# Kernel optimization log

Measured on AMD Instinct MI355X. Metric: run time of the kernel, lower is better.

## Reference

```python
import jax, jax.numpy as jnp
import numpy as np

NUM_NODES = 102400
NUM_EDGES = 3276800
NUM_GRAPHS = 1024
LAMBDA_MAX = 2.0


def setup_inputs() -> dict:
    key = jax.random.key(0)
    ks = jax.random.split(key, 12)
    inp = {}
    inp['x'] = jax.random.normal(ks[0], (NUM_NODES, 128), dtype=jnp.float32)
    inp['edge_index'] = jax.random.randint(ks[1], (2, NUM_EDGES), 0, NUM_NODES, dtype=jnp.int32).astype(jnp.int64)
    inp['edge_attr'] = jax.random.uniform(ks[2], (NUM_EDGES,), dtype=jnp.float32)
    inp['batch'] = jnp.sort(jax.random.randint(ks[3], (NUM_NODES,), 0, NUM_GRAPHS, dtype=jnp.int32).astype(jnp.int64))
    inp['w1'] = jax.random.normal(ks[4], (3, 128, 64), dtype=jnp.float32) * 0.05
    inp['b1'] = jax.random.normal(ks[5], (64,), dtype=jnp.float32) * 0.05
    inp['w2'] = jax.random.normal(ks[6], (3, 64, 64), dtype=jnp.float32) * 0.05
    inp['b2'] = jax.random.normal(ks[7], (64,), dtype=jnp.float32) * 0.05
    inp['w3'] = jax.random.normal(ks[8], (3, 64, 128), dtype=jnp.float32) * 0.05
    inp['b3'] = jax.random.normal(ks[9], (128,), dtype=jnp.float32) * 0.05
    inp['lin_w'] = jax.random.normal(ks[10], (128, 2), dtype=jnp.float32) * 0.05
    inp['lin_b'] = jax.random.normal(ks[11], (2,), dtype=jnp.float32) * 0.05
    return inp


def _cheb_norm(edge_index, edge_attr, num_nodes):
    # PyG ChebConv.__norm__ with normalization='sym', lambda_max=2.0:
    #   L = I - D^{-1/2} A D^{-1/2};  Lhat = (2/lambda_max) * L - I
    # off-diagonal weights: -(2/lmax) * d_i^{-1/2} w_ij d_j^{-1/2}
    # diagonal coefficient:  (2/lmax) - 1  (== 0 for lmax = 2)
    src, dst = edge_index[0], edge_index[1]
    deg = jax.ops.segment_sum(edge_attr, src, num_segments=num_nodes)
    dinv = jnp.where(deg > 0, jax.lax.rsqrt(jnp.where(deg > 0, deg, 1.0)), 0.0)
    w = -(2.0 / LAMBDA_MAX) * dinv[src] * edge_attr * dinv[dst]
    diag = (2.0 / LAMBDA_MAX) - 1.0
    return w, diag


def _cheb_conv(x, src, dst, norm_w, diag, weight, bias):
    # weight: [K, Fin, Fout]; Chebyshev recurrence T0=x, T1=Lhat x, Tk=2 Lhat T_{k-1} - T_{k-2}
    n = x.shape[0]

    def spmv(v):  # Lhat @ v via edge-list scatter/gather
        return jax.ops.segment_sum(norm_w[:, None] * v[src], dst, num_segments=n) + diag * v

    Tx0 = x
    out = Tx0 @ weight[0]
    Tx1 = spmv(Tx0)
    out = out + Tx1 @ weight[1]
    for k in range(2, weight.shape[0]):
        Tx2 = 2.0 * spmv(Tx1) - Tx0
        out = out + Tx2 @ weight[k]
        Tx0, Tx1 = Tx1, Tx2
    return out + bias


def reference(x, edge_index, edge_attr, batch, w1, b1, w2, b2, w3, b3, lin_w, lin_b):
    n = x.shape[0]
    src, dst = edge_index[0], edge_index[1]
    norm_w, diag = _cheb_norm(edge_index, edge_attr, n)
    h = jax.nn.relu(_cheb_conv(x, src, dst, norm_w, diag, w1, b1))
    h = jax.nn.relu(_cheb_conv(h, src, dst, norm_w, diag, w2, b2))
    h = jax.nn.relu(_cheb_conv(h, src, dst, norm_w, diag, w3, b3))
    # global_mean_pool over graph ids
    sums = jax.ops.segment_sum(h, batch, num_segments=NUM_GRAPHS)
    cnts = jax.ops.segment_sum(jnp.ones((n,), h.dtype), batch, num_segments=NUM_GRAPHS)
    pooled = sums / jnp.maximum(cnts, 1.0)[:, None]
    return pooled @ lin_w + lin_b
```

## Files before the change

### kernel.cpp

```cpp
#include <hip/hip_runtime.h>
#include <cstddef>
#include <cstdint>

#define N_NODES 102400
#define N_EDGES 3276800
#define N_GRAPHS 1024
#define NBUCK 400
#define NBB 512
#define EPB 6400
#define MAXB 12288
#define N64 ((size_t)N_NODES * 64)

typedef unsigned short ushortT;
typedef unsigned int uintT;
typedef __attribute__((ext_vector_type(8))) short bf16x8;
typedef __attribute__((ext_vector_type(4))) float f32x4;

__device__ __forceinline__ float b2f(ushortT h) {
    return __uint_as_float(((uintT)h) << 16);
}
__device__ __forceinline__ ushortT f2b(float f) {
    uintT u = __float_as_uint(f);
    uintT r = (u + 0x7fffu + ((u >> 16) & 1u)) >> 16;
    return (ushortT)r;
}
__device__ __forceinline__ float loF(uintT w) { return __uint_as_float(w << 16); }
__device__ __forceinline__ float hiF(uintT w) { return __uint_as_float(w & 0xffff0000u); }

__global__ __launch_bounds__(256) void k_binA(const int* __restrict__ src,
                                              const int* __restrict__ dst,
                                              int* __restrict__ blkCntD,
                                              int* __restrict__ blkCntS) {
    __shared__ int hd[NBUCK], hs[NBUCK];
    int t = threadIdx.x;
    for (int i = t; i < NBUCK; i += 256) { hd[i] = 0; hs[i] = 0; }
    __syncthreads();
    int base = blockIdx.x * EPB;
    const int4* s4 = (const int4*)(src + base);
    const int4* d4 = (const int4*)(dst + base);
    for (int v = t; v < EPB / 4; v += 256) {
        int4 d = d4[v];
        int4 s = s4[v];
        atomicAdd(&hd[d.x >> 8], 1);
        atomicAdd(&hd[d.y >> 8], 1);
        atomicAdd(&hd[d.z >> 8], 1);
        atomicAdd(&hd[d.w >> 8], 1);
        atomicAdd(&hs[s.x >> 8], 1);
        atomicAdd(&hs[s.y >> 8], 1);
        atomicAdd(&hs[s.z >> 8], 1);
        atomicAdd(&hs[s.w >> 8], 1);
    }
    __syncthreads();
    for (int i = t; i < NBUCK; i += 256) {
        blkCntD[(size_t)blockIdx.x * NBUCK + i] = hd[i];
        blkCntS[(size_t)blockIdx.x * NBUCK + i] = hs[i];
    }
}

__global__ __launch_bounds__(256) void k_bbase(const int* __restrict__ blkCnt,
                                               int* __restrict__ blkRel,
                                               int* __restrict__ bucketTot) {
    __shared__ int sc[NBB];
    int b = blockIdx.x, t = threadIdx.x;
    int v0 = blkCnt[(size_t)t * NBUCK + b];
    int v1 = blkCnt[(size_t)(t + 256) * NBUCK + b];
    sc[t] = v0; sc[t + 256] = v1;
    __syncthreads();
    for (int o = 1; o < NBB; o <<= 1) {
        int x0 = (t >= o) ? sc[t - o] : 0;
        int x1 = (t + 256 >= o) ? sc[t + 256 - o] : 0;
        __syncthreads();
        sc[t] += x0; sc[t + 256] += x1;
        __syncthreads();
    }
    blkRel[(size_t)t * NBUCK + b] = sc[t] - v0;
    blkRel[(size_t)(t + 256) * NBUCK + b] = sc[t + 256] - v1;
    if (t == 255) bucketTot[b] = sc[NBB - 1];
}

__global__ void k_bscan(const int* __restrict__ bucketTotD,
                        const int* __restrict__ bucketTotS,
                        int* __restrict__ binBaseD,
                        int* __restrict__ binBaseS,
                        int* __restrict__ rowp) {
    int t = threadIdx.x;
    if (t == 0) {
        int run = 0;
        for (int i = 0; i < NBUCK; i++) { binBaseD[i] = run; run += bucketTotD[i]; }
        binBaseD[NBUCK] = run;
        rowp[N_NODES] = run;
    } else if (t == 64) {
        int run = 0;
        for (int i = 0; i < NBUCK; i++) { binBaseS[i] = run; run += bucketTotS[i]; }
        binBaseS[NBUCK] = run;
    }
}

__global__ __launch_bounds__(512) void k_binB2(const int* __restrict__ src,
                                               const int* __restrict__ dst,
                                               const float* __restrict__ attr,
                                               const int* __restrict__ blkCntD,
                                               const int* __restrict__ blkCntS,
                                               const int* __restrict__ blkRelD,
                                               const int* __restrict__ blkRelS,
                                               const int* __restrict__ binBaseD,
                                               const int* __restrict__ binBaseS,
                                               int2* __restrict__ edsD,
                                               int2* __restrict__ edsS) {
    __shared__ int sxD[EPB];
    __shared__ int syD[EPB];
    __shared__ ushortT spD[EPB];
    __shared__ int sxS[EPB];
    __shared__ int syS[EPB];
    __shared__ ushortT spS[EPB];
    __shared__ int lcurD[NBUCK], deltaD[NBUCK];
    __shared__ int lcurS[NBUCK], deltaS[NBUCK];
    int bx = blockIdx.x, t = threadIdx.x;

    int vD = (t < NBUCK) ? blkCntD[(size_t)bx * NBUCK + t] : 0;
    int vS = (t < NBUCK) ? blkCntS[(size_t)bx * NBUCK + t] : 0;
    sxD[t] = vD; sxS[t] = vS;
    __syncthreads();
    for (int o = 1; o < 512; o <<= 1) {
        int xD = (t >= o) ? sxD[t - o] : 0;
        int xS = (t >= o) ? sxS[t - o] : 0;
        __syncthreads();
        sxD[t] += xD; sxS[t] += xS;
        __syncthreads();
    }
    if (t < NBUCK) {
        int eD = sxD[t] - vD;
        lcurD[t] = eD;
        deltaD[t] = binBaseD[t] + blkRelD[(size_t)bx * NBUCK + t] - eD;
        int eS = sxS[t] - vS;
        lcurS[t] = eS;
        deltaS[t] = binBaseS[t] + blkRelS[(size_t)bx * NBUCK + t] - eS;
    }
    __syncthreads();

    int base = bx * EPB;
    for (int v = t; v < EPB / 2; v += 512) {
        int e0 = base + v * 2;
        int2 s2 = *(const int2*)(src + e0);
        int2 d2 = *(const int2*)(dst + e0);
        float2 a2 = *(const float2*)(attr + e0);
        int bkt, lp;
        bkt = d2.x >> 8;
        lp = atomicAdd(&lcurD[bkt], 1);
        spD[lp] = (ushortT)bkt; sxD[lp] = (s2.x << 8) | (d2.x & 255);
        syD[lp] = __float_as_int(a2.x);
        bkt = s2.x >> 8;
        lp = atomicAdd(&lcurS[bkt], 1);
        spS[lp] = (ushortT)bkt; sxS[lp] = s2.x & 255;
        syS[lp] = __float_as_int(a2.x);
        bkt = d2.y >> 8;
        lp = atomicAdd(&lcurD[bkt], 1);
        spD[lp] = (ushortT)bkt; sxD[lp] = (s2.y << 8) | (d2.y & 255);
        syD[lp] = __float_as_int(a2.y);
        bkt = s2.y >> 8;
        lp = atomicAdd(&lcurS[bkt], 1);
        spS[lp] = (ushortT)bkt; sxS[lp] = s2.y & 255;
        syS[lp] = __float_as_int(a2.y);
    }
    __syncthreads();
    for (int i = t; i < EPB; i += 512) {
        edsD[i + deltaD[spD[i]]] = make_int2(sxD[i], syD[i]);
        edsS[i + deltaS[spS[i]]] = make_int2(sxS[i], syS[i]);
    }
}

__global__ __launch_bounds__(256) void k_deg(const int2* __restrict__ edsS,
                                             const int* __restrict__ binBaseS,
                                             float* __restrict__ dinv) {
    __shared__ float degL[256];
    int b = blockIdx.x, t = threadIdx.x;
    degL[t] = 0.f;
    __syncthreads();
    int s0 = binBaseS[b], s1 = binBaseS[b + 1];
    for (int i = s0 + t; i < s1; i += 256) {
        int2 e = edsS[i];
        atomicAdd(&degL[e.x], __int_as_float(e.y));
    }
    __syncthreads();
    float d = degL[t];
    dinv[b * 256 + t] = d > 0.f ? rsqrtf(d) : 0.f;
}

__global__ __launch_bounds__(512) void k_csr(const int2* __restrict__ edsD,
                                             const int* __restrict__ binBaseD,
                                             const float* __restrict__ dinvG,
                                             int* __restrict__ rowp,
                                             int2* __restrict__ cedge) {
    __shared__ int cnt2[256 * 16];
    __shared__ int cntL[256];
    __shared__ float dL[256];
    __shared__ int2 st[MAXB];
    int b = blockIdx.x, t = threadIdx.x;
    for (int i = t; i < 256 * 16; i += 512) cnt2[i] = 0;
    if (t < 256) dL[t] = dinvG[b * 256 + t];
    __syncthreads();
    int s0 = binBaseD[b], s1 = binBaseD[b + 1];
    for (int i = s0 + t; i < s1; i += 512) {
        int2 e = edsD[i];
        atomicAdd(&cnt2[(e.x & 255) * 16 + ((e.x >> 8) >> 13)], 1);
    }
    __syncthreads();
    if (t < 256) {
        int run = 0;
#pragma unroll
        for (int o = 0; o < 16; o++) {
            int c = cnt2[t * 16 + o];
            cnt2[t * 16 + o] = run;
            run += c;
        }
        cntL[t] = run;
    }
    __syncthreads();
    int v = (t < 256) ? cntL[t] : 0;
    for (int o = 1; o < 256; o <<= 1) {
        int x = (t < 256 && t >= o) ? cntL[t - o] : 0;
        __syncthreads();
        if (t < 256) cntL[t] += x;
        __syncthreads();
    }
    if (t < 256) {
        int excl = cntL[t] - v;
        rowp[b * 256 + t] = s0 + excl;
#pragma unroll
        for (int o = 0; o < 16; o++) cnt2[t * 16 + o] += excl;
    }
    __syncthreads();
    for (int i = s0 + t; i < s1; i += 512) {
        int2 e = edsD[i];
        int dl = e.x & 255;
        int sg = e.x >> 8;
        float w = -__int_as_float(e.y) * dinvG[sg] * dL[dl];
        int p = atomicAdd(&cnt2[dl * 16 + (sg >> 13)], 1);
        st[p] = make_int2(sg, __float_as_int(w));
    }
    __syncthreads();
    int n = s1 - s0;
    for (int i = t; i < n; i += 512) cedge[s0 + i] = st[i];
}

__global__ __launch_bounds__(256) void k_cast(const float* __restrict__ x,
                                              ushortT* __restrict__ Xhi,
                                              ushortT* __restrict__ Xlo) {
    int i = blockIdx.x * 256 + threadIdx.x;
    int n = i >> 5;
    int kq = (i & 31) * 4;
    float4 v = ((const float4*)x)[i];
    int s = kq >> 6, kk = kq & 63;
    size_t o = (size_t)s * N64 + (size_t)n * 64 + kk;
    ushort4 h, l;
    h.x = f2b(v.x); l.x = f2b(v.x - b2f(h.x));
    h.y = f2b(v.y); l.y = f2b(v.y - b2f(h.y));
    h.z = f2b(v.z); l.z = f2b(v.z - b2f(h.z));
    h.w = f2b(v.w); l.w = f2b(v.w - b2f(h.w));
    *(ushort4*)(Xhi + o) = h;
    *(ushort4*)(Xlo + o) = l;
}

template <int L>
__global__ void k_wprep(const float* __restrict__ w, ushortT* __restrict__ Wth,
                        ushortT* __restrict__ Wtl) {
    int i = blockIdx.x * 256 + threadIdx.x;
    float v;
    if (L == 1) {
        if (i >= 192 * 128) return;
        int n = i / 128, k = i % 128;
        if (n < 64)       v = w[k * 64 + n] - w[16384 + k * 64 + n];
        else if (n < 128) v = w[8192 + k * 64 + (n - 64)];
        else              v = w[16384 + k * 64 + (n - 128)];
    } else if (L == 2) {
        if (i >= 192 * 64) return;
        int n = i / 64, k = i % 64;
        if (n < 64)       v = w[k * 64 + n] - w[8192 + k * 64 + n];
        else if (n < 128) v = w[4096 + k * 64 + (n - 64)];
        else              v = w[8192 + k * 64 + (n - 128)];
    } else {
        if (i >= 128 * 192) return;
        int n = i / 192, k = i % 192;
        v = w[(k >> 6) * 8192 + (k & 63) * 128 + n];
    }
    ushortT h = f2b(v);
    Wth[i] = h;
    Wtl[i] = f2b(v - b2f(h));
}

template <int KTOT, int NTOT, int MODE>
__global__ __launch_bounds__(512) void k_mgemm(
    const ushortT* __restrict__ Ah0, const ushortT* __restrict__ Ah1,
    const ushortT* __restrict__ Ah2, const ushortT* __restrict__ Al0,
    const ushortT* __restrict__ Al1, const ushortT* __restrict__ Al2,
    const ushortT* __restrict__ Wth, const ushortT* __restrict__ Wtl,
    const float* __restrict__ bias, float* __restrict__ outf,
    ushortT* __restrict__ outb) {
    constexpr int KPAD = 72;
    constexpr int NCT = NTOT / 16;
    __shared__ ushortT Bh[NTOT * KPAD];
    __shared__ ushortT Bl[NTOT * KPAD];
    const ushortT* Ah[3] = {Ah0, Ah1, Ah2};
    const ushortT* Al[3] = {Al0, Al1, Al2};
    int t = threadIdx.x;
    int lane = t & 63;
    int wv = t >> 6;
    int m = lane & 15, q = lane >> 4;
    int r0 = blockIdx.x * 256 + wv * 32;
    int ar0 = r0 + m;
    int ar1 = r0 + 16 + m;

    f32x4 acc[2][NCT];
#pragma unroll
    for (int rf = 0; rf < 2; rf++)
#pragma unroll
        for (int ct = 0; ct < NCT; ct++)
#pragma unroll
            for (int j = 0; j < 4; j++) acc[rf][ct][j] = 0.f;

#pragma unroll
    for (int kc = 0; kc < KTOT / 64; kc++) {
        __syncthreads();
        for (int i = t; i < NTOT * 8; i += 512) {
            int col = i >> 3, k = (i & 7) * 8;
            *(uint4*)(Bh + col * KPAD + k) =
                *(const uint4*)(Wth + (size_t)col * KTOT + kc * 64 + k);
            *(uint4*)(Bl + col * KPAD + k) =
                *(const uint4*)(Wtl + (size_t)col * KTOT + kc * 64 + k);
        }
        __syncthreads();
        const ushortT* Ahc = Ah[kc];
        const ushortT* Alc = Al[kc];
#pragma unroll
        for (int ks2 = 0; ks2 < 2; ks2++) {
            int kk = ks2 * 32 + q * 8;
            bf16x8 ah0 = *(const bf16x8*)(Ahc + (size_t)ar0 * 64 + kk);
            bf16x8 al0 = *(const bf16x8*)(Alc + (size_t)ar0 * 64 + kk);
            bf16x8 ah1 = *(const bf16x8*)(Ahc + (size_t)ar1 * 64 + kk);
            bf16x8 al1 = *(const bf16x8*)(Alc + (size_t)ar1 * 64 + kk);
#pragma unroll
            for (int ct = 0; ct < NCT; ct++) {
                int bo = (ct * 16 + m) * KPAD + ks2 * 32 + q * 8;
                bf16x8 bh = *(const bf16x8*)(Bh + bo);
                bf16x8 bl = *(const bf16x8*)(Bl + bo);
                acc[0][ct] = __builtin_amdgcn_mfma_f32_16x16x32_bf16(ah0, bh, acc[0][ct], 0, 0, 0);
                acc[0][ct] = __builtin_amdgcn_mfma_f32_16x16x32_bf16(al0, bh, acc[0][ct], 0, 0, 0);
                acc[0][ct] = __builtin_amdgcn_mfma_f32_16x16x32_bf16(ah0, bl, acc[0][ct], 0, 0, 0);
                acc[1][ct] = __builtin_amdgcn_mfma_f32_16x16x32_bf16(ah1, bh, acc[1][ct], 0, 0, 0);
                acc[1][ct] = __builtin_amdgcn_mfma_f32_16x16x32_bf16(al1, bh, acc[1][ct], 0, 0, 0);
                acc[1][ct] = __builtin_amdgcn_mfma_f32_16x16x32_bf16(ah1, bl, acc[1][ct], 0, 0, 0);
            }
        }
    }

#pragma unroll
    for (int rf = 0; rf < 2; rf++)
#pragma unroll
        for (int ct = 0; ct < NCT; ct++)
#pragma unroll
            for (int rg = 0; rg < 4; rg++) {
                int row = r0 + rf * 16 + q * 4 + rg;
                float v = acc[rf][ct][rg];
                if (MODE == 0) {
                    if (ct < 8)
                        outf[(size_t)row * 128 + ct * 16 + m] = v;
                    else
                        outb[(size_t)row * 64 + (ct - 8) * 16 + m] = f2b(v);
                } else {
                    int col = ct * 16 + m;
                    outf[(size_t)row * 128 + col] = fmaxf(v + bias[col], 0.f);
                }
            }
}

template <int MODE, int SA, bool AUXB, bool WLO>
__global__ __launch_bounds__(256) void k_spmm(const int* __restrict__ rowp,
                                              const int2* __restrict__ cedge,
                                              const ushortT* __restrict__ Xb,
                                              const float* __restrict__ auxF,
                                              const ushortT* __restrict__ auxH,
                                              const ushortT* __restrict__ auxL,
                                              const float* __restrict__ bias,
                                              ushortT* __restrict__ Yh,
                                              ushortT* __restrict__ Yl) {
    int node = blockIdx.x * 4 + (threadIdx.x >> 6);
    int lane = threadIdx.x & 63;
    int q = lane >> 3;
    int f = (lane & 7) * 8;
    int s = rowp[node], e = rowp[node + 1];
    const ushortT* Xf = Xb + f;
    float a0 = 0.f, a1 = 0.f, a2 = 0.f, a3 = 0.f;
    float a4 = 0.f, a5 = 0.f, a6 = 0.f, a7 = 0.f;
    for (int i = s; i < e; i += 16) {
        int i0 = min(i + q, e - 1);
        int i1 = min(i + 8 + q, e - 1);
        int2 ed0 = cedge[i0];
        int2 ed1 = cedge[i1];
        float w0 = (i + q < e) ? __int_as_float(ed0.y) : 0.f;
        float w1 = (i + 8 + q < e) ? __int_as_float(ed1.y) : 0.f;
        uint4 u0 = *(const uint4*)(Xf + ((size_t)ed0.x << 6));
        uint4 u1 = *(const uint4*)(Xf + ((size_t)ed1.x << 6));
        a0 = fmaf(w0, loF(u0.x), a0);
        a1 = fmaf(w0, hiF(u0.x), a1);
        a2 = fmaf(w0, loF(u0.y), a2);
        a3 = fmaf(w0, hiF(u0.y), a3);
        a4 = fmaf(w0, loF(u0.z), a4);
        a5 = fmaf(w0, hiF(u0.z), a5);
        a6 = fmaf(w0, loF(u0.w), a6);
        a7 = fmaf(w0, hiF(u0.w), a7);
        a0 = fmaf(w1, loF(u1.x), a0);
        a1 = fmaf(w1, hiF(u1.x), a1);
        a2 = fmaf(w1, loF(u1.y), a2);
        a3 = fmaf(w1, hiF(u1.y), a3);
        a4 = fmaf(w1, loF(u1.z), a4);
        a5 = fmaf(w1, hiF(u1.z), a5);
        a6 = fmaf(w1, loF(u1.w), a6);
        a7 = fmaf(w1, hiF(u1.w), a7);
    }
    a0 += __shfl_xor(a0, 8); a0 += __shfl_xor(a0, 16); a0 += __shfl_xor(a0, 32);
    a1 += __shfl_xor(a1, 8); a1 += __shfl_xor(a1, 16); a1 += __shfl_xor(a1, 32);
    a2 += __shfl_xor(a2, 8); a2 += __shfl_xor(a2, 16); a2 += __shfl_xor(a2, 32);
    a3 += __shfl_xor(a3, 8); a3 += __shfl_xor(a3, 16); a3 += __shfl_xor(a3, 32);
    a4 += __shfl_xor(a4, 8); a4 += __shfl_xor(a4, 16); a4 += __shfl_xor(a4, 32);
    a5 += __shfl_xor(a5, 8); a5 += __shfl_xor(a5, 16); a5 += __shfl_xor(a5, 32);
    a6 += __shfl_xor(a6, 8); a6 += __shfl_xor(a6, 16); a6 += __shfl_xor(a6, 32);
    a7 += __shfl_xor(a7, 8); a7 += __shfl_xor(a7, 16); a7 += __shfl_xor(a7, 32);

    if (q == 0 || (WLO && q == 1)) {
        float x0 = 0.f, x1 = 0.f, x2 = 0.f, x3 = 0.f;
        float x4 = 0.f, x5 = 0.f, x6 = 0.f, x7 = 0.f;
        if (MODE != 0) {
            if (AUXB) {
                uint4 ha = *(const uint4*)(auxH + (size_t)node * 64 + f);
                uint4 la = *(const uint4*)(auxL + (size_t)node * 64 + f);
                x0 = loF(ha.x) + loF(la.x);
                x1 = hiF(ha.x) + hiF(la.x);
                x2 = loF(ha.y) + loF(la.y);
                x3 = hiF(ha.y) + hiF(la.y);
                x4 = loF(ha.z) + loF(la.z);
                x5 = hiF(ha.z) + hiF(la.z);
                x6 = loF(ha.w) + loF(la.w);
                x7 = hiF(ha.w) + hiF(la.w);
            } else {
                float4 av0 = *(const float4*)(auxF + (size_t)node * SA + f);
                float4 av1 = *(const float4*)(auxF + (size_t)node * SA + f + 4);
                x0 = av0.x; x1 = av0.y; x2 = av0.z; x3 = av0.w;
                x4 = av1.x; x5 = av1.y; x6 = av1.z; x7 = av1.w;
            }
        }
        float r0, r1, r2, r3, r4, r5, r6, r7;
        if (MODE == 0) {
            r0 = a0; r1 = a1; r2 = a2; r3 = a3;
            r4 = a4; r5 = a5; r6 = a6; r7 = a7;
        } else if (MODE == 1) {
            r0 = x0 + 2.f * a0; r1 = x1 + 2.f * a1;
            r2 = x2 + 2.f * a2; r3 = x3 + 2.f * a3;
            r4 = x4 + 2.f * a4; r5 = x5 + 2.f * a5;
            r6 = x6 + 2.f * a6; r7 = x7 + 2.f * a7;
        } else if (MODE == 2) {
            r0 = 2.f * a0 - x0; r1 = 2.f * a1 - x1;
            r2 = 2.f * a2 - x2; r3 = 2.f * a3 - x3;
            r4 = 2.f * a4 - x4; r5 = 2.f * a5 - x5;
            r6 = 2.f * a6 - x6; r7 = 2.f * a7 - x7;
        } else {
            float4 bv0 = *(const float4*)(bias + f);
            float4 bv1 = *(const float4*)(bias + f + 4);
            r0 = fmaxf(x0 + a0 + bv0.x, 0.f);
            r1 = fmaxf(x1 + a1 + bv0.y, 0.f);
            r2 = fmaxf(x2 + a2 + bv0.z, 0.f);
            r3 = fmaxf(x3 + a3 + bv0.w, 0.f);
            r4 = fmaxf(x4 + a4 + bv1.x, 0.f);
            r5 = fmaxf(x5 + a5 + bv1.y, 0.f);
            r6 = fmaxf(x6 + a6 + bv1.z, 0.f);
            r7 = fmaxf(x7 + a7 + bv1.w, 0.f);
        }
        ushortT h0 = f2b(r0), h1 = f2b(r1), h2 = f2b(r2), h3 = f2b(r3);
        ushortT h4 = f2b(r4), h5 = f2b(r5), h6 = f2b(r6), h7 = f2b(r7);
        if (q == 0) {
            uint4 pk;
            pk.x = (uintT)h0 | ((uintT)h1 << 16);
            pk.y = (uintT)h2 | ((uintT)h3 << 16);
            pk.z = (uintT)h4 | ((uintT)h5 << 16);
            pk.w = (uintT)h6 | ((uintT)h7 << 16);
            *(uint4*)(Yh + (size_t)node * 64 + f) = pk;
        } else {
            uint4 pk;
            pk.x = (uintT)f2b(r0 - b2f(h0)) | ((uintT)f2b(r1 - b2f(h1)) << 16);
            pk.y = (uintT)f2b(r2 - b2f(h2)) | ((uintT)f2b(r3 - b2f(h3)) << 16);
            pk.z = (uintT)f2b(r4 - b2f(h4)) | ((uintT)f2b(r5 - b2f(h5)) << 16);
            pk.w = (uintT)f2b(r6 - b2f(h6)) | ((uintT)f2b(r7 - b2f(h7)) << 16);
            *(uint4*)(Yl + (size_t)node * 64 + f) = pk;
        }
    }
}

__global__ __launch_bounds__(128) void k_pool(const int* __restrict__ batch,
                                              const float* __restrict__ H3,
                                              float* __restrict__ pooled,
                                              float* __restrict__ gcnt) {
    int t = threadIdx.x;
    int n0 = blockIdx.x * 64;
    int g = batch[n0];
    float a = 0.f;
    int c = 0;
    for (int k = 0; k < 64; k++) {
        int gn = batch[n0 + k];
        if (gn != g) {
            atomicAdd(&pooled[(size_t)g * 128 + t], a);
            if (t == 0) atomicAdd(&gcnt[g], (float)c);
            g = gn; a = 0.f; c = 0;
        }
        a += H3[(size_t)(n0 + k) * 128 + t];
        c++;
    }
    atomicAdd(&pooled[(size_t)g * 128 + t], a);
    if (t == 0) atomicAdd(&gcnt[g], (float)c);
}

__global__ void k_final(const float* __restrict__ pooled, const float* __restrict__ gcnt,
                        const float* __restrict__ lin_w, const float* __restrict__ lin_b,
                        float* __restrict__ out) {
    int g = blockIdx.x * 4 + (threadIdx.x >> 6);
    int lane = threadIdx.x & 63;
    if (g >= N_GRAPHS) return;
    float inv = 1.f / fmaxf(gcnt[g], 1.f);
    float v0 = pooled[(size_t)g * 128 + lane] * inv;
    float v1 = pooled[(size_t)g * 128 + 64 + lane] * inv;
    float p0 = v0 * lin_w[lane * 2 + 0] + v1 * lin_w[(lane + 64) * 2 + 0];
    float p1 = v0 * lin_w[lane * 2 + 1] + v1 * lin_w[(lane + 64) * 2 + 1];
    for (int o = 32; o > 0; o >>= 1) {
        p0 += __shfl_down(p0, o);
        p1 += __shfl_down(p1, o);
    }
    if (lane == 0) {
        out[g * 2 + 0] = p0 + lin_b[0];
        out[g * 2 + 1] = p1 + lin_b[1];
    }
}

extern "C" void kernel_launch(void* const* d_in, const int* in_sizes, int n_in,
                              void* d_out, int out_size, void* d_ws, size_t ws_size,
                              hipStream_t stream) {
    const float* x     = (const float*)d_in[0];
    const int*   src   = (const int*)d_in[1];
    const int*   dst   = src + N_EDGES;
    const float* eattr = (const float*)d_in[2];
    const int*   batch = (const int*)d_in[3];
    const float* w1    = (const float*)d_in[4];
    const float* b1    = (const float*)d_in[5];
    const float* w2    = (const float*)d_in[6];
    const float* b2    = (const float*)d_in[7];
    const float* w3    = (const float*)d_in[8];
    const float* b3    = (const float*)d_in[9];
    const float* lin_w = (const float*)d_in[10];
    const float* lin_b = (const float*)d_in[11];
    float* out = (float*)d_out;

    char* ws = (char*)d_ws;
    size_t off = 0;
    auto alloc = [&](size_t bytes) -> char* {
        char* p = ws + off;
        off += (bytes + 255) & ~(size_t)255;
        return p;
    };
    int*   blkCntD   = (int*)  alloc((size_t)NBB * NBUCK * 4);
    int*   blkCntS   = (int*)  alloc((size_t)NBB * NBUCK * 4);
    int*   blkRelD   = (int*)  alloc((size_t)NBB * NBUCK * 4);
    int*   blkRelS   = (int*)  alloc((size_t)NBB * NBUCK * 4);
    int*   bucketTotD = (int*) alloc(NBUCK * 4);
    int*   bucketTotS = (int*) alloc(NBUCK * 4);
    int*   binBaseD  = (int*)  alloc((NBUCK + 1) * 4);
    int*   binBaseS  = (int*)  alloc((NBUCK + 1) * 4);
    float* dinv      = (float*)alloc((size_t)N_NODES * 4);
    int*   rowp      = (int*)  alloc((size_t)(N_NODES + 1) * 4);
    ushortT* Wt1h   = (ushortT*)alloc(192 * 128 * 2);
    ushortT* Wt1l   = (ushortT*)alloc(192 * 128 * 2);
    ushortT* Wt2h   = (ushortT*)alloc(192 * 64 * 2);
    ushortT* Wt2l   = (ushortT*)alloc(192 * 64 * 2);
    ushortT* Wt3h   = (ushortT*)alloc(128 * 192 * 2);
    ushortT* Wt3l   = (ushortT*)alloc(128 * 192 * 2);
    float* pooled   = (float*)alloc((size_t)(N_GRAPHS * 128 + N_GRAPHS) * 4);
    float* gcnt     = pooled + (size_t)N_GRAPHS * 128;
    int2*  cedge    = (int2*) alloc((size_t)N_EDGES * 8);
    char*  Buf1     = alloc((size_t)N_EDGES * 16);
    char*  Buf2     = alloc((size_t)N_NODES * 128 * 4);
    char*  Buf3     = alloc(4 * N64 * 2);

    int2* edsD = (int2*)Buf1;
    int2* edsS = edsD + N_EDGES;
    ushortT* Xhi  = (ushortT*)Buf1;
    ushortT* Xlo  = Xhi + 2 * N64;
    ushortT* GThi = (ushortT*)Buf1;
    float* P  = (float*)Buf2;
    float* H3 = (float*)Buf2;
    ushortT* G0    = (ushortT*)Buf3;
    ushortT* Qhi   = G0 + N64;
    ushortT* H1hi  = G0 + 2 * N64;
    ushortT* H1lo  = G0 + 3 * N64;
    ushortT* GTlo0 = G0;
    ushortT* GTlo1 = H1hi;
    ushortT* GTlo2 = H1lo;

    hipMemsetAsync(pooled, 0, (size_t)(N_GRAPHS * 128 + N_GRAPHS) * 4, stream);

    k_binA<<<NBB, 256, 0, stream>>>(src, dst, blkCntD, blkCntS);
    k_bbase<<<NBUCK, 256, 0, stream>>>(blkCntD, blkRelD, bucketTotD);
    k_bbase<<<NBUCK, 256, 0, stream>>>(blkCntS, blkRelS, bucketTotS);
    k_bscan<<<1, 128, 0, stream>>>(bucketTotD, bucketTotS, binBaseD, binBaseS, rowp);
    k_binB2<<<NBB, 512, 0, stream>>>(src, dst, eattr, blkCntD, blkCntS,
                                     blkRelD, blkRelS, binBaseD, binBaseS,
                                     edsD, edsS);
    k_deg<<<NBUCK, 256, 0, stream>>>(edsS, binBaseS, dinv);
    k_csr<<<NBUCK, 512, 0, stream>>>(edsD, binBaseD, dinv, rowp, cedge);

    k_cast<<<N_NODES * 32 / 256, 256, 0, stream>>>(x, Xhi, Xlo);
    k_wprep<1><<<96, 256, 0, stream>>>(w1, Wt1h, Wt1l);
    k_wprep<2><<<48, 256, 0, stream>>>(w2, Wt2h, Wt2l);
    k_wprep<3><<<96, 256, 0, stream>>>(w3, Wt3h, Wt3l);

    k_mgemm<128, 192, 0><<<N_NODES / 256, 512, 0, stream>>>(
        Xhi, Xhi + N64, nullptr, Xlo, Xlo + N64, nullptr, Wt1h, Wt1l, nullptr, P, G0);
    k_spmm<1, 128, false, false><<<N_NODES / 4, 256, 0, stream>>>(
        rowp, cedge, G0, P + 64, nullptr, nullptr, nullptr, Qhi, nullptr);
    k_spmm<3, 128, false, true><<<N_NODES / 4, 256, 0, stream>>>(
        rowp, cedge, Qhi, P, nullptr, nullptr, b1, H1hi, H1lo);

    k_mgemm<64, 192, 0><<<N_NODES / 256, 512, 0, stream>>>(
        H1hi, nullptr, nullptr, H1lo, nullptr, nullptr, Wt2h, Wt2l, nullptr, P, G0);
    k_spmm<1, 128, false, false><<<N_NODES / 4, 256, 0, stream>>>(
        rowp, cedge, G0, P + 64, nullptr, nullptr, nullptr, Qhi, nullptr);
    k_spmm<3, 128, false, true><<<N_NODES / 4, 256, 0, stream>>>(
        rowp, cedge, Qhi, P, nullptr, nullptr, b2, GThi, GTlo0);

    k_spmm<0, 64, false, true><<<N_NODES / 4, 256, 0, stream>>>(
        rowp, cedge, GThi, nullptr, nullptr, nullptr, nullptr, GThi + N64, GTlo1);
    k_spmm<2, 64, true, true><<<N_NODES / 4, 256, 0, stream>>>(
        rowp, cedge, GThi + N64, nullptr, GThi, GTlo0, nullptr, GThi + 2 * N64, GTlo2);
    k_mgemm<192, 128, 1><<<N_NODES / 256, 512, 0, stream>>>(
        GThi, GThi + N64, GThi + 2 * N64, GTlo0, GTlo1, GTlo2, Wt3h, Wt3l, b3, H3, nullptr);

    k_pool<<<N_NODES / 64, 128, 0, stream>>>(batch, H3, pooled, gcnt);
    k_final<<<N_GRAPHS / 4, 256, 0, stream>>>(pooled, gcnt, lin_w, lin_b, out);
}
```

Before: 739.1 us.

## Fuse mean-pool into final GEMM epilogue and double edge-binning blocks

The last MFMA GEMM now stages its ReLU output tile in shared memory and reduces it per graph segment with atomics, which removes the separate pooling kernel and the 52MB H3 write and read. Shared memory is reused as a union of the weight stage and a 128KB pool buffer, and that larger allocation may lower occupancy for the final GEMM. Separately, the edge-binning block count doubles with half the edges per block, and the block-base scan is widened to 512 threads to match.

```diff
diff --git a/kernel.cpp b/kernel.cpp
--- a/kernel.cpp
+++ b/kernel.cpp
@@ -6,8 +6,8 @@
 #define N_EDGES 3276800
 #define N_GRAPHS 1024
 #define NBUCK 400
-#define NBB 512
-#define EPB 6400
+#define NBB 1024
+#define EPB 3200
 #define MAXB 12288
 #define N64 ((size_t)N_NODES * 64)
 
@@ -57,25 +57,25 @@
     }
 }
 
-__global__ __launch_bounds__(256) void k_bbase(const int* __restrict__ blkCnt,
+__global__ __launch_bounds__(512) void k_bbase(const int* __restrict__ blkCnt,
                                                int* __restrict__ blkRel,
                                                int* __restrict__ bucketTot) {
     __shared__ int sc[NBB];
     int b = blockIdx.x, t = threadIdx.x;
     int v0 = blkCnt[(size_t)t * NBUCK + b];
-    int v1 = blkCnt[(size_t)(t + 256) * NBUCK + b];
-    sc[t] = v0; sc[t + 256] = v1;
+    int v1 = blkCnt[(size_t)(t + 512) * NBUCK + b];
+    sc[t] = v0; sc[t + 512] = v1;
     __syncthreads();
     for (int o = 1; o < NBB; o <<= 1) {
         int x0 = (t >= o) ? sc[t - o] : 0;
-        int x1 = (t + 256 >= o) ? sc[t + 256 - o] : 0;
-        __syncthreads();
-        sc[t] += x0; sc[t + 256] += x1;
+        int x1 = (t + 512 >= o) ? sc[t + 512 - o] : 0;
+        __syncthreads();
+        sc[t] += x0; sc[t + 512] += x1;
         __syncthreads();
     }
     blkRel[(size_t)t * NBUCK + b] = sc[t] - v0;
-    blkRel[(size_t)(t + 256) * NBUCK + b] = sc[t + 256] - v1;
-    if (t == 255) bucketTot[b] = sc[NBB - 1];
+    blkRel[(size_t)(t + 512) * NBUCK + b] = sc[t + 512] - v1;
+    if (t == 511) bucketTot[b] = sc[NBB - 1];
 }
 
 __global__ void k_bscan(const int* __restrict__ bucketTotD,
@@ -295,11 +295,16 @@
     const ushortT* __restrict__ Al1, const ushortT* __restrict__ Al2,
     const ushortT* __restrict__ Wth, const ushortT* __restrict__ Wtl,
     const float* __restrict__ bias, float* __restrict__ outf,
-    ushortT* __restrict__ outb) {
+    ushortT* __restrict__ outb, const int* __restrict__ batch,
+    float* __restrict__ pooled, float* __restrict__ gcnt) {
     constexpr int KPAD = 72;
     constexpr int NCT = NTOT / 16;
-    __shared__ ushortT Bh[NTOT * KPAD];
-    __shared__ ushortT Bl[NTOT * KPAD];
+    constexpr int SMEM_STAGE = 2 * NTOT * KPAD * 2;
+    constexpr int SMEM_POOL = (MODE == 1) ? (256 * 128 * 4 + 256 * 4) : 0;
+    constexpr int SMEM_BYTES = SMEM_STAGE > SMEM_POOL ? SMEM_STAGE : SMEM_POOL;
+    __shared__ __align__(16) char smem[SMEM_BYTES];
+    ushortT* Bh = (ushortT*)smem;
+    ushortT* Bl = Bh + NTOT * KPAD;
     const ushortT* Ah[3] = {Ah0, Ah1, Ah2};
     const ushortT* Al[3] = {Al0, Al1, Al2};
     int t = threadIdx.x;
@@ -353,24 +358,55 @@
         }
     }
 
-#pragma unroll
-    for (int rf = 0; rf < 2; rf++)
-#pragma unroll
-        for (int ct = 0; ct < NCT; ct++)
-#pragma unroll
-            for (int rg = 0; rg < 4; rg++) {
-                int row = r0 + rf * 16 + q * 4 + rg;
-                float v = acc[rf][ct][rg];
-                if (MODE == 0) {
+    if (MODE == 0) {
+#pragma unroll
+        for (int rf = 0; rf < 2; rf++)
+#pragma unroll
+            for (int ct = 0; ct < NCT; ct++)
+#pragma unroll
+                for (int rg = 0; rg < 4; rg++) {
+                    int row = r0 + rf * 16 + q * 4 + rg;
+                    float v = acc[rf][ct][rg];
                     if (ct < 8)
                         outf[(size_t)row * 128 + ct * 16 + m] = v;
                     else
                         outb[(size_t)row * 64 + (ct - 8) * 16 + m] = f2b(v);
-                } else {
+                }
+    } else {
+        float* poolB = (float*)smem;
+        int* batchL = (int*)(smem + 256 * 128 * 4);
+        __syncthreads();
+        for (int i = t; i < 256; i += 512)
+            batchL[i] = batch[blockIdx.x * 256 + i];
+#pragma unroll
+        for (int rf = 0; rf < 2; rf++)
+#pragma unroll
+            for (int ct = 0; ct < NCT; ct++)
+#pragma unroll
+                for (int rg = 0; rg < 4; rg++) {
+                    int rl = wv * 32 + rf * 16 + q * 4 + rg;
                     int col = ct * 16 + m;
-                    outf[(size_t)row * 128 + col] = fmaxf(v + bias[col], 0.f);
+                    poolB[rl * 128 + col] = fmaxf(acc[rf][ct][rg] + bias[col], 0.f);
                 }
+        __syncthreads();
+        int col = t & 127, seg = t >> 7;
+        int base = seg * 64;
+        int g = batchL[base];
+        float a = 0.f;
+        int c = 0;
+        for (int k = 0; k < 64; k++) {
+            int gn = batchL[base + k];
+            if (gn != g) {
+                atomicAdd(&pooled[(size_t)g * 128 + col], a);
+                if (col == 0) atomicAdd(&gcnt[g], (float)c);
+                g = gn; a = 0.f; c = 0;
             }
+            a += poolB[(base + k) * 128 + col];
+            c++;
+        }
+        atomicAdd(&pooled[(size_t)g * 128 + col], a);
+        if (col == 0) atomicAdd(&gcnt[g], (float)c);
+    }
 }
 
 template <int MODE, int SA, bool AUXB, bool WLO>
@@ -494,29 +530,6 @@
     }
 }
 
-__global__ __launch_bounds__(128) void k_pool(const int* __restrict__ batch,
-                                              const float* __restrict__ H3,
-                                              float* __restrict__ pooled,
-                                              float* __restrict__ gcnt) {
-    int t = threadIdx.x;
-    int n0 = blockIdx.x * 64;
-    int g = batch[n0];
-    float a = 0.f;
-    int c = 0;
-    for (int k = 0; k < 64; k++) {
-        int gn = batch[n0 + k];
-        if (gn != g) {
-            atomicAdd(&pooled[(size_t)g * 128 + t], a);
-            if (t == 0) atomicAdd(&gcnt[g], (float)c);
-            g = gn; a = 0.f; c = 0;
-        }
-        a += H3[(size_t)(n0 + k) * 128 + t];
-        c++;
-    }
-    atomicAdd(&pooled[(size_t)g * 128 + t], a);
-    if (t == 0) atomicAdd(&gcnt[g], (float)c);
-}
-
 __global__ void k_final(const float* __restrict__ pooled, const float* __restrict__ gcnt,
                         const float* __restrict__ lin_w, const float* __restrict__ lin_b,
                         float* __restrict__ out) {
@@ -592,7 +605,6 @@
     ushortT* Xlo  = Xhi + 2 * N64;
     ushortT* GThi = (ushortT*)Buf1;
     float* P  = (float*)Buf2;
-    float* H3 = (float*)Buf2;
     ushortT* G0    = (ushortT*)Buf3;
     ushortT* Qhi   = G0 + N64;
     ushortT* H1hi  = G0 + 2 * N64;
@@ -604,8 +616,8 @@
     hipMemsetAsync(pooled, 0, (size_t)(N_GRAPHS * 128 + N_GRAPHS) * 4, stream);
 
     k_binA<<<NBB, 256, 0, stream>>>(src, dst, blkCntD, blkCntS);
-    k_bbase<<<NBUCK, 256, 0, stream>>>(blkCntD, blkRelD, bucketTotD);
-    k_bbase<<<NBUCK, 256, 0, stream>>>(blkCntS, blkRelS, bucketTotS);
+    k_bbase<<<NBUCK, 512, 0, stream>>>(blkCntD, blkRelD, bucketTotD);
+    k_bbase<<<NBUCK, 512, 0, stream>>>(blkCntS, blkRelS, bucketTotS);
     k_bscan<<<1, 128, 0, stream>>>(bucketTotD, bucketTotS, binBaseD, binBaseS, rowp);
     k_binB2<<<NBB, 512, 0, stream>>>(src, dst, eattr, blkCntD, blkCntS,
                                      blkRelD, blkRelS, binBaseD, binBaseS,
@@ -619,14 +631,16 @@
     k_wprep<3><<<96, 256, 0, stream>>>(w3, Wt3h, Wt3l);
 
     k_mgemm<128, 192, 0><<<N_NODES / 256, 512, 0, stream>>>(
-        Xhi, Xhi + N64, nullptr, Xlo, Xlo + N64, nullptr, Wt1h, Wt1l, nullptr, P, G0);
+        Xhi, Xhi + N64, nullptr, Xlo, Xlo + N64, nullptr, Wt1h, Wt1l, nullptr,
+        P, G0, nullptr, nullptr, nullptr);
     k_spmm<1, 128, false, false><<<N_NODES / 4, 256, 0, stream>>>(
         rowp, cedge, G0, P + 64, nullptr, nullptr, nullptr, Qhi, nullptr);
     k_spmm<3, 128, false, true><<<N_NODES / 4, 256, 0, stream>>>(
         rowp, cedge, Qhi, P, nullptr, nullptr, b1, H1hi, H1lo);
 
     k_mgemm<64, 192, 0><<<N_NODES / 256, 512, 0, stream>>>(
-        H1hi, nullptr, nullptr, H1lo, nullptr, nullptr, Wt2h, Wt2l, nullptr, P, G0);
+        H1hi, nullptr, nullptr, H1lo, nullptr, nullptr, Wt2h, Wt2l, nullptr,
+        P, G0, nullptr, nullptr, nullptr);
     k_spmm<1, 128, false, false><<<N_NODES / 4, 256, 0, stream>>>(
         rowp, cedge, G0, P + 64, nullptr, nullptr, nullptr, Qhi, nullptr);
     k_spmm<3, 128, false, true><<<N_NODES / 4, 256, 0, stream>>>(
@@ -637,8 +651,8 @@
     k_spmm<2, 64, true, true><<<N_NODES / 4, 256, 0, stream>>>(
         rowp, cedge, GThi + N64, nullptr, GThi, GTlo0, nullptr, GThi + 2 * N64, GTlo2);
     k_mgemm<192, 128, 1><<<N_NODES / 256, 512, 0, stream>>>(
-        GThi, GThi + N64, GThi + 2 * N64, GTlo0, GTlo1, GTlo2, Wt3h, Wt3l, b3, H3, nullptr);
-
-    k_pool<<<N_NODES / 64, 128, 0, stream>>>(batch, H3, pooled, gcnt);
+        GThi, GThi + N64, GThi + 2 * N64, GTlo0, GTlo1, GTlo2, Wt3h, Wt3l, b3,
+        nullptr, nullptr, batch, pooled, gcnt);
+
     k_final<<<N_GRAPHS / 4, 256, 0, stream>>>(pooled, gcnt, lin_w, lin_b, out);
 }
```

Result: no change. 727.4 us (-1.6%).
